# Optimization experiments

Measured on AMD Instinct MI355X. Metric: run time of the kernel, lower is better.

## Reference

```python
import jax, jax.numpy as jnp
import numpy as np

N_HIT = 50000
N_TRUE = 512
N_EDGE = 40000
D = 8
S_B = 1.0
Q_MIN = 0.5


def setup_inputs() -> dict:
    key = jax.random.key(0)
    k_x, k_f, k_y, k_eh, k_ep = jax.random.split(key, 5)
    x = jax.random.normal(k_x, (N_HIT, D), dtype=jnp.float32)
    # f is a sigmoid-like filter output in (0,1); keep away from 1 so atanh is finite
    f = jax.random.uniform(k_f, (N_HIT,), dtype=jnp.float32, minval=0.01, maxval=0.95)
    # y == -1 marks background hits; otherwise an instance id
    y = jax.random.randint(k_y, (N_HIT,), -1, N_TRUE, dtype=jnp.int64)
    e_h = jax.random.randint(k_eh, (N_EDGE,), 0, N_HIT, dtype=jnp.int64)
    e_p = jax.random.randint(k_ep, (N_EDGE,), 0, N_TRUE, dtype=jnp.int64)
    # guarantee every true particle has at least one assigned hit
    e_p = e_p.at[:N_TRUE].set(jnp.arange(N_TRUE, dtype=jnp.int64))
    return {"x": x, "f": f, "y": y, "e_h": e_h, "e_p": e_p}


def reference(x, f, y, e_h, e_p):
    n_hit = x.shape[0]
    fe = f[e_h]  # [n_edge]
    # scatter_max with zero-initialized output: clamp below at 0
    f_centers = jax.ops.segment_max(fe, e_p, num_segments=N_TRUE)
    f_centers = jnp.maximum(f_centers, 0.0)  # [n_true]
    # argmax hit per particle: among edges attaining the segment max, take largest hit id
    is_max = fe == f_centers[e_p]
    centers = jax.ops.segment_max(jnp.where(is_max, e_h, -1), e_p, num_segments=N_TRUE)  # [n_true]

    bkg_mask = y == -1
    n_bkg = bkg_mask.sum().astype(f.dtype)

    b1 = 1.0 - f_centers.sum() / N_TRUE
    b2 = S_B / n_bkg * jnp.where(bkg_mask, f, 0.0).sum()

    q = jnp.square(jnp.arctanh(f)) + Q_MIN  # [n_hit]

    # membership mask m_ik [n_hit, n_true]
    m_ik = jnp.zeros((n_hit, N_TRUE), dtype=bool).at[e_h, e_p].set(True)

    # pairwise squared distances to condensation centers [n_hit, n_true]
    xc = x[centers]  # [n_true, d]
    dist = jnp.sum(jnp.square(x[:, None, :] - xc[None, :, :]), axis=2)

    # attractive inside instance, hinged repulsive outside
    v = jnp.where(m_ik, dist, jnp.clip(1.0 - dist, 0.0))
    v = (jnp.sum(v * q[centers][None, :], axis=1) * q).sum() / n_hit

    return jnp.stack([b1 + b2, v])
```

## Files before the change

### kernel.cpp

```cpp
#include <hip/hip_runtime.h>
#include <math.h>

#define N_HIT  50000
#define N_TRUE 512
#define N_EDGE 40000
#define Q_MIN  0.5f

#define W_SEG     0
#define W_DONE    1024
#define W_VPART   1040
#define W_BKGF    2048
#define W_BKGN    2560
#define W_QARR    4096

#define K1_GRID   512
#define KSPLIT    32
#define KCH       (N_TRUE / KSPLIT)
#define HPT       13
#define HCHUNK    (256 * HPT)
#define NHB       16
#define G2        (NHB * KSPLIT)
#define HPB       98
#define EPB       79

#define AG_LDF(p) __hip_atomic_load((p), __ATOMIC_RELAXED, __HIP_MEMORY_SCOPE_AGENT)

__global__ __launch_bounds__(256) void k1(const float* __restrict__ f,
                                          const int* __restrict__ y,
                                          const int* __restrict__ e_h,
                                          const int* __restrict__ e_p,
                                          unsigned* __restrict__ ws) {
    const int t = threadIdx.x, b = blockIdx.x;
    unsigned long long* __restrict__ seg = (unsigned long long*)ws;
    float* __restrict__ wsf = (float*)ws;

    float sf = 0.f;
    bool isb = false;
    if (t < HPB) {
        const int i = b * HPB + t;
        if (i < N_HIT) {
            const float fi = f[i];
            const float a  = atanhf(fi);
            wsf[W_QARR + i] = fmaf(a, a, Q_MIN);
            isb = (y[i] == -1);
            if (isb) sf = fi;
        }
    } else if (t >= 128 && t < 128 + EPB) {
        const int e = b * EPB + (t - 128);
        if (e < N_EDGE) {
            const int h = e_h[e], p = e_p[e];
            const unsigned long long packed = 0x8000000000000000ull |
                ((unsigned long long)__float_as_uint(f[h]) << 32) | (unsigned)h;
            atomicMax(&seg[p], packed);
        }
    }
    for (int off = 32; off; off >>= 1) sf += __shfl_down(sf, off, 64);
    const unsigned long long bal = __ballot(isb);
    __shared__ float r[8];
    if ((t & 63) == 0) { r[t >> 6] = sf; r[4 + (t >> 6)] = (float)__popcll(bal); }
    __syncthreads();
    if (t == 0) {
        wsf[W_BKGF + b] = r[0] + r[1] + r[2] + r[3];
        wsf[W_BKGN + b] = r[4] + r[5] + r[6] + r[7];
    }
    if (b == 0 && t < 9) {
        const int slot[9] = {W_DONE, W_VPART, W_VPART + 16, W_VPART + 32,
                             W_VPART + 48, W_VPART + 64, W_VPART + 80,
                             W_VPART + 96, W_VPART + 112};
        ws[slot[t]] = 0u;
    }
}

__global__ __launch_bounds__(256, 2) void k2(const float* __restrict__ x,
                                             const int* __restrict__ e_h,
                                             const int* __restrict__ e_p,
                                             unsigned* __restrict__ ws,
                                             float* __restrict__ out) {
    const int t = threadIdx.x, b = blockIdx.x;
    const unsigned long long* __restrict__ seg = (const unsigned long long*)ws;
    const float* __restrict__ wsf = (const float*)ws;
    const int kb = b & (KSPLIT - 1);
    const int hb = b >> 5;

    __shared__ float ct[KCH * 12];
    __shared__ float r[4];
    if (t < KCH) {
        const unsigned long long w = seg[kb * KCH + t];
        const int c = (int)(unsigned)w;
        const float4* xp = (const float4*)(x + (size_t)c * 8);
        const float4 x0 = xp[0], x1 = xp[1];
        float c2 = x0.x * x0.x;
        c2 = fmaf(x0.y, x0.y, c2); c2 = fmaf(x0.z, x0.z, c2);
        c2 = fmaf(x0.w, x0.w, c2); c2 = fmaf(x1.x, x1.x, c2);
        c2 = fmaf(x1.y, x1.y, c2); c2 = fmaf(x1.z, x1.z, c2);
        c2 = fmaf(x1.w, x1.w, c2);
        *(float4*)(ct + 12 * t)     = make_float4(2.f * x0.x, 2.f * x0.y,
                                                  2.f * x0.z, 2.f * x0.w);
        *(float4*)(ct + 12 * t + 4) = make_float4(2.f * x1.x, 2.f * x1.y,
                                                  2.f * x1.z, 2.f * x1.w);
        ct[12 * t + 8] = 1.f - c2;
        ct[12 * t + 9] = wsf[W_QARR + c];
    }

    float4 xr0[HPT], xr1[HPT];
    float  xi2v[HPT], qiv[HPT], acc[HPT];
#pragma unroll
    for (int j = 0; j < HPT; ++j) {
        const int i = hb * HCHUNK + j * 256 + t;
        const bool valid = (i < N_HIT);
        const int  ic = valid ? i : 0;
        const float4* xp = (const float4*)(x + (size_t)ic * 8);
        xr0[j] = xp[0]; xr1[j] = xp[1];
        float s = xr0[j].x * xr0[j].x;
        s = fmaf(xr0[j].y, xr0[j].y, s); s = fmaf(xr0[j].z, xr0[j].z, s);
        s = fmaf(xr0[j].w, xr0[j].w, s); s = fmaf(xr1[j].x, xr1[j].x, s);
        s = fmaf(xr1[j].y, xr1[j].y, s); s = fmaf(xr1[j].z, xr1[j].z, s);
        s = fmaf(xr1[j].w, xr1[j].w, s);
        xi2v[j] = s;
        qiv[j]  = valid ? wsf[W_QARR + i] : 0.f;
        acc[j]  = 0.f;
    }
    __syncthreads();

#pragma unroll
    for (int k2i = 0; k2i < KCH; ++k2i) {
        const float4 c0  = *(const float4*)(ct + 12 * k2i);
        const float4 c1  = *(const float4*)(ct + 12 * k2i + 4);
        const float  tk  = ct[12 * k2i + 8];
        const float  qck = ct[12 * k2i + 9];
#pragma unroll
        for (int j = 0; j < HPT; ++j) {
            float s = tk - xi2v[j];
            s = fmaf(xr0[j].x, c0.x, s); s = fmaf(xr0[j].y, c0.y, s);
            s = fmaf(xr0[j].z, c0.z, s); s = fmaf(xr0[j].w, c0.w, s);
            s = fmaf(xr1[j].x, c1.x, s); s = fmaf(xr1[j].y, c1.y, s);
            s = fmaf(xr1[j].z, c1.z, s); s = fmaf(xr1[j].w, c1.w, s);
            const float rep = fmaxf(s, 0.f);
            acc[j] = fmaf(rep, qck, acc[j]);
        }
    }
    float vout = 0.f;
#pragma unroll
    for (int j = 0; j < HPT; ++j) vout = fmaf(acc[j], qiv[j], vout);

    if (t < EPB) {
        const int e = b * EPB + t;
        if (e < N_EDGE) {
            const int h = e_h[e], p = e_p[e];
            const int c = (int)(unsigned)seg[p];
            const float4* hp4 = (const float4*)(x + (size_t)h * 8);
            const float4 a0 = hp4[0], a1 = hp4[1];
            const float4* cp4 = (const float4*)(x + (size_t)c * 8);
            const float4 c0 = cp4[0], c1 = cp4[1];
            float dot = a0.x * c0.x, xh2 = a0.x * a0.x, xc2 = c0.x * c0.x;
            dot = fmaf(a0.y, c0.y, dot); xh2 = fmaf(a0.y, a0.y, xh2); xc2 = fmaf(c0.y, c0.y, xc2);
            dot = fmaf(a0.z, c0.z, dot); xh2 = fmaf(a0.z, a0.z, xh2); xc2 = fmaf(c0.z, c0.z, xc2);
            dot = fmaf(a0.w, c0.w, dot); xh2 = fmaf(a0.w, a0.w, xh2); xc2 = fmaf(c0.w, c0.w, xc2);
            dot = fmaf(a1.x, c1.x, dot); xh2 = fmaf(a1.x, a1.x, xh2); xc2 = fmaf(c1.x, c1.x, xc2);
            dot = fmaf(a1.y, c1.y, dot); xh2 = fmaf(a1.y, a1.y, xh2); xc2 = fmaf(c1.y, c1.y, xc2);
            dot = fmaf(a1.z, c1.z, dot); xh2 = fmaf(a1.z, a1.z, xh2); xc2 = fmaf(c1.z, c1.z, xc2);
            dot = fmaf(a1.w, c1.w, dot); xh2 = fmaf(a1.w, a1.w, xh2); xc2 = fmaf(c1.w, c1.w, xc2);
            const float dist  = fmaf(-2.f, dot, xh2 + xc2);
            const float hinge = fmaxf(1.f - dist, 0.f);
            const float qh = wsf[W_QARR + h];
            const float qc = wsf[W_QARR + c];
            vout = fmaf(qh * qc, dist - hinge, vout);
        }
    }

    for (int off = 32; off; off >>= 1) vout += __shfl_down(vout, off, 64);
    if ((t & 63) == 0) r[t >> 6] = vout;
    __syncthreads();

    __shared__ int last;
    if (t == 0) {
        atomicAdd((float*)wsf + W_VPART + (b & 7) * 16, r[0] + r[1] + r[2] + r[3]);
        __threadfence();
        last = (atomicAdd(&ws[W_DONE], 1u) == G2 - 1);
    }
    __syncthreads();
    if (!last) return;
    __threadfence();

    float lfc = __uint_as_float((unsigned)(__hip_atomic_load(&seg[t], __ATOMIC_RELAXED,
                  __HIP_MEMORY_SCOPE_AGENT) >> 32) & 0x7FFFFFFFu)
              + __uint_as_float((unsigned)(__hip_atomic_load(&seg[t + 256], __ATOMIC_RELAXED,
                  __HIP_MEMORY_SCOPE_AGENT) >> 32) & 0x7FFFFFFFu);
    float lbf = AG_LDF(wsf + W_BKGF + t) + AG_LDF(wsf + W_BKGF + t + 256);
    float lbn = AG_LDF(wsf + W_BKGN + t) + AG_LDF(wsf + W_BKGN + t + 256);
    for (int off = 32; off; off >>= 1) {
        lfc += __shfl_down(lfc, off, 64);
        lbf += __shfl_down(lbf, off, 64);
        lbn += __shfl_down(lbn, off, 64);
    }
    __shared__ float fr[12];
    if ((t & 63) == 0) {
        fr[t >> 6] = lfc; fr[4 + (t >> 6)] = lbf; fr[8 + (t >> 6)] = lbn;
    }
    __syncthreads();
    if (t == 0) {
        float vs = 0.f;
        for (int s = 0; s < 8; ++s)
            vs += AG_LDF(wsf + W_VPART + s * 16);
        const float sum_fc  = fr[0] + fr[1] + fr[2] + fr[3];
        const float sum_bkg = fr[4] + fr[5] + fr[6] + fr[7];
        const float nb      = fr[8] + fr[9] + fr[10] + fr[11];
        out[0] = (1.f - sum_fc / (float)N_TRUE) + sum_bkg / nb;
        out[1] = vs / (float)N_HIT;
    }
}

extern "C" void kernel_launch(void* const* d_in, const int* in_sizes, int n_in,
                              void* d_out, int out_size, void* d_ws, size_t ws_size,
                              hipStream_t stream) {
    const float* x   = (const float*)d_in[0];
    const float* f   = (const float*)d_in[1];
    const int*   y   = (const int*)d_in[2];
    const int*   e_h = (const int*)d_in[3];
    const int*   e_p = (const int*)d_in[4];
    float* out = (float*)d_out;
    unsigned* ws = (unsigned*)d_ws;

    k1<<<K1_GRID, 256, 0, stream>>>(f, y, e_h, e_p, ws);
    k2<<<G2, 256, 0, stream>>>(x, e_h, e_p, ws, out);
}
```

Before: 89.78 us.

## Fuse both kernels into one persistent kernel with grid barrier

Merges the segment-max/background pass and the distance pass into a single 512-block launch. An atomic spin barrier replaces the kernel boundary. The q array is recomputed with atanhf where needed instead of being stored to workspace. This removes one launch and the q round trip through memory. In exchange it adds a spin barrier that requires all blocks to be co-resident, and its counters assume the workspace starts at a fixed poison value.

```diff
diff --git a/kernel.cpp b/kernel.cpp
--- a/kernel.cpp
+++ b/kernel.cpp
@@ -5,87 +5,98 @@
 #define N_TRUE 512
 #define N_EDGE 40000
 #define Q_MIN  0.5f
+#define POISON 0xAAAAAAAAu
 
 #define W_SEG     0
 #define W_DONE    1024
-#define W_VPART   1040
+#define W_BAR     1056
+#define W_VPART   1072
 #define W_BKGF    2048
 #define W_BKGN    2560
-#define W_QARR    4096
-
-#define K1_GRID   512
+
 #define KSPLIT    32
 #define KCH       (N_TRUE / KSPLIT)
 #define HPT       13
 #define HCHUNK    (256 * HPT)
-#define NHB       16
-#define G2        (NHB * KSPLIT)
+#define GRID      512
 #define HPB       98
 #define EPB       79
 
 #define AG_LDF(p) __hip_atomic_load((p), __ATOMIC_RELAXED, __HIP_MEMORY_SCOPE_AGENT)
 
-__global__ __launch_bounds__(256) void k1(const float* __restrict__ f,
-                                          const int* __restrict__ y,
-                                          const int* __restrict__ e_h,
-                                          const int* __restrict__ e_p,
-                                          unsigned* __restrict__ ws) {
+__global__ __launch_bounds__(256, 2) void fused(const float* __restrict__ x,
+                                                const float* __restrict__ f,
+                                                const int* __restrict__ y,
+                                                const int* __restrict__ e_h,
+                                                const int* __restrict__ e_p,
+                                                unsigned* __restrict__ ws,
+                                                float* __restrict__ out) {
     const int t = threadIdx.x, b = blockIdx.x;
     unsigned long long* __restrict__ seg = (unsigned long long*)ws;
     float* __restrict__ wsf = (float*)ws;
-
+    const int kb = b & (KSPLIT - 1);
+    const int hb = b >> 5;
+
+    __shared__ float ct[KCH * 12];
+    __shared__ float r[8];
+
+    if (t < EPB) {
+        const int e = b * EPB + t;
+        if (e < N_EDGE) {
+            const int h = e_h[e], p = e_p[e];
+            const unsigned long long packed = 0x8000000000000000ull |
+                ((unsigned long long)__float_as_uint(f[h]) << 32) | (unsigned)h;
+            atomicMax(&seg[p], packed);
+        }
+    }
     float sf = 0.f;
     bool isb = false;
     if (t < HPB) {
         const int i = b * HPB + t;
         if (i < N_HIT) {
             const float fi = f[i];
-            const float a  = atanhf(fi);
-            wsf[W_QARR + i] = fmaf(a, a, Q_MIN);
             isb = (y[i] == -1);
             if (isb) sf = fi;
         }
-    } else if (t >= 128 && t < 128 + EPB) {
-        const int e = b * EPB + (t - 128);
-        if (e < N_EDGE) {
-            const int h = e_h[e], p = e_p[e];
-            const unsigned long long packed = 0x8000000000000000ull |
-                ((unsigned long long)__float_as_uint(f[h]) << 32) | (unsigned)h;
-            atomicMax(&seg[p], packed);
-        }
-    }
+    }
+    if (b == 0 && t < 8) ws[W_VPART + t * 16] = 0u;
+
+    float4 xr0[HPT], xr1[HPT];
+    float  qiv[HPT];
+#pragma unroll
+    for (int j = 0; j < HPT; ++j) {
+        const int i  = hb * HCHUNK + j * 256 + t;
+        const bool valid = (i < N_HIT);
+        const int  ic = valid ? i : 0;
+        const float4* xp = (const float4*)(x + (size_t)ic * 8);
+        xr0[j] = xp[0]; xr1[j] = xp[1];
+        if (valid) {
+            const float a = atanhf(f[i]);
+            qiv[j] = fmaf(a, a, Q_MIN);
+        } else {
+            qiv[j] = 0.f;
+        }
+    }
+
     for (int off = 32; off; off >>= 1) sf += __shfl_down(sf, off, 64);
     const unsigned long long bal = __ballot(isb);
-    __shared__ float r[8];
     if ((t & 63) == 0) { r[t >> 6] = sf; r[4 + (t >> 6)] = (float)__popcll(bal); }
     __syncthreads();
     if (t == 0) {
         wsf[W_BKGF + b] = r[0] + r[1] + r[2] + r[3];
         wsf[W_BKGN + b] = r[4] + r[5] + r[6] + r[7];
-    }
-    if (b == 0 && t < 9) {
-        const int slot[9] = {W_DONE, W_VPART, W_VPART + 16, W_VPART + 32,
-                             W_VPART + 48, W_VPART + 64, W_VPART + 80,
-                             W_VPART + 96, W_VPART + 112};
-        ws[slot[t]] = 0u;
-    }
-}
-
-__global__ __launch_bounds__(256, 2) void k2(const float* __restrict__ x,
-                                             const int* __restrict__ e_h,
-                                             const int* __restrict__ e_p,
-                                             unsigned* __restrict__ ws,
-                                             float* __restrict__ out) {
-    const int t = threadIdx.x, b = blockIdx.x;
-    const unsigned long long* __restrict__ seg = (const unsigned long long*)ws;
-    const float* __restrict__ wsf = (const float*)ws;
-    const int kb = b & (KSPLIT - 1);
-    const int hb = b >> 5;
-
-    __shared__ float ct[KCH * 12];
-    __shared__ float r[4];
+        __threadfence();
+        __hip_atomic_fetch_add(&ws[W_BAR], 1u, __ATOMIC_RELEASE,
+                               __HIP_MEMORY_SCOPE_AGENT);
+        while (__hip_atomic_load(&ws[W_BAR], __ATOMIC_ACQUIRE,
+                                 __HIP_MEMORY_SCOPE_AGENT) - POISON < GRID)
+            __builtin_amdgcn_s_sleep(1);
+        __threadfence();
+    }
+    __syncthreads();
+
     if (t < KCH) {
-        const unsigned long long w = seg[kb * KCH + t];
+        const unsigned long long w = AG_LDF(&seg[kb * KCH + t]);
         const int c = (int)(unsigned)w;
         const float4* xp = (const float4*)(x + (size_t)c * 8);
         const float4 x0 = xp[0], x1 = xp[1];
@@ -99,25 +110,18 @@
         *(float4*)(ct + 12 * t + 4) = make_float4(2.f * x1.x, 2.f * x1.y,
                                                   2.f * x1.z, 2.f * x1.w);
         ct[12 * t + 8] = 1.f - c2;
-        ct[12 * t + 9] = wsf[W_QARR + c];
-    }
-
-    float4 xr0[HPT], xr1[HPT];
-    float  xi2v[HPT], qiv[HPT], acc[HPT];
+        const float ac = atanhf(f[c]);
+        ct[12 * t + 9] = fmaf(ac, ac, Q_MIN);
+    }
+    float xi2v[HPT], acc[HPT];
 #pragma unroll
     for (int j = 0; j < HPT; ++j) {
-        const int i = hb * HCHUNK + j * 256 + t;
-        const bool valid = (i < N_HIT);
-        const int  ic = valid ? i : 0;
-        const float4* xp = (const float4*)(x + (size_t)ic * 8);
-        xr0[j] = xp[0]; xr1[j] = xp[1];
         float s = xr0[j].x * xr0[j].x;
         s = fmaf(xr0[j].y, xr0[j].y, s); s = fmaf(xr0[j].z, xr0[j].z, s);
         s = fmaf(xr0[j].w, xr0[j].w, s); s = fmaf(xr1[j].x, xr1[j].x, s);
         s = fmaf(xr1[j].y, xr1[j].y, s); s = fmaf(xr1[j].z, xr1[j].z, s);
         s = fmaf(xr1[j].w, xr1[j].w, s);
         xi2v[j] = s;
-        qiv[j]  = valid ? wsf[W_QARR + i] : 0.f;
         acc[j]  = 0.f;
     }
     __syncthreads();
@@ -147,7 +151,7 @@
         const int e = b * EPB + t;
         if (e < N_EDGE) {
             const int h = e_h[e], p = e_p[e];
-            const int c = (int)(unsigned)seg[p];
+            const int c = (int)(unsigned)AG_LDF(&seg[p]);
             const float4* hp4 = (const float4*)(x + (size_t)h * 8);
             const float4 a0 = hp4[0], a1 = hp4[1];
             const float4* cp4 = (const float4*)(x + (size_t)c * 8);
@@ -162,30 +166,31 @@
             dot = fmaf(a1.w, c1.w, dot); xh2 = fmaf(a1.w, a1.w, xh2); xc2 = fmaf(c1.w, c1.w, xc2);
             const float dist  = fmaf(-2.f, dot, xh2 + xc2);
             const float hinge = fmaxf(1.f - dist, 0.f);
-            const float qh = wsf[W_QARR + h];
-            const float qc = wsf[W_QARR + c];
+            const float ah = atanhf(f[h]);
+            const float af = atanhf(f[c]);
+            const float qh = fmaf(ah, ah, Q_MIN);
+            const float qc = fmaf(af, af, Q_MIN);
             vout = fmaf(qh * qc, dist - hinge, vout);
         }
     }
 
     for (int off = 32; off; off >>= 1) vout += __shfl_down(vout, off, 64);
+    __syncthreads();
     if ((t & 63) == 0) r[t >> 6] = vout;
     __syncthreads();
 
     __shared__ int last;
     if (t == 0) {
-        atomicAdd((float*)wsf + W_VPART + (b & 7) * 16, r[0] + r[1] + r[2] + r[3]);
+        atomicAdd(wsf + W_VPART + (b & 7) * 16, r[0] + r[1] + r[2] + r[3]);
         __threadfence();
-        last = (atomicAdd(&ws[W_DONE], 1u) == G2 - 1);
+        last = (atomicAdd(&ws[W_DONE], 1u) == POISON + GRID - 1);
     }
     __syncthreads();
     if (!last) return;
     __threadfence();
 
-    float lfc = __uint_as_float((unsigned)(__hip_atomic_load(&seg[t], __ATOMIC_RELAXED,
-                  __HIP_MEMORY_SCOPE_AGENT) >> 32) & 0x7FFFFFFFu)
-              + __uint_as_float((unsigned)(__hip_atomic_load(&seg[t + 256], __ATOMIC_RELAXED,
-                  __HIP_MEMORY_SCOPE_AGENT) >> 32) & 0x7FFFFFFFu);
+    float lfc = __uint_as_float((unsigned)(AG_LDF(&seg[t]) >> 32) & 0x7FFFFFFFu)
+              + __uint_as_float((unsigned)(AG_LDF(&seg[t + 256]) >> 32) & 0x7FFFFFFFu);
     float lbf = AG_LDF(wsf + W_BKGF + t) + AG_LDF(wsf + W_BKGF + t + 256);
     float lbn = AG_LDF(wsf + W_BKGN + t) + AG_LDF(wsf + W_BKGN + t + 256);
     for (int off = 32; off; off >>= 1) {
@@ -221,6 +226,5 @@
     float* out = (float*)d_out;
     unsigned* ws = (unsigned*)d_ws;
 
-    k1<<<K1_GRID, 256, 0, stream>>>(f, y, e_h, e_p, ws);
-    k2<<<G2, 256, 0, stream>>>(x, e_h, e_p, ws, out);
+    fused<<<GRID, 256, 0, stream>>>(x, f, y, e_h, e_p, ws, out);
 }
```

Result: slower. 152.7 us (+70.1%).
